# Kernel optimization log

Measured on AMD Instinct MI355X. Metric: run time of the kernel, lower is better.

The kernel has to match this reference:

```python
import jax, jax.numpy as jnp
import numpy as np

D_MODEL = 256
NUM_HEADS = 8
DEPTH = D_MODEL // NUM_HEADS
CITY_SEQ = 2048
B = 4
SQ = 2048
EPS = 1e-9
WEIGHTING = 'IDW'  # branch used (Linear/IDW/Gaussian in original)


def setup_inputs() -> dict:
    key = jax.random.key(0)
    ks = jax.random.split(key, 12)
    s = 1.0 / np.sqrt(D_MODEL)
    return {
        'query': jax.random.normal(ks[0], (B, SQ, D_MODEL), jnp.float32),
        'values': jax.random.normal(ks[1], (B, SQ, D_MODEL), jnp.float32),
        'distance_matrix': jax.random.uniform(ks[2], (B, SQ, CITY_SEQ), jnp.float32),
        'Wq_w': jax.random.normal(ks[3], (D_MODEL, D_MODEL), jnp.float32) * s,
        'Wq_b': jnp.zeros((D_MODEL,), jnp.float32),
        'Wk_w': jax.random.normal(ks[4], (D_MODEL, D_MODEL), jnp.float32) * s,
        'Wk_b': jnp.zeros((D_MODEL,), jnp.float32),
        'Wv_w': jax.random.normal(ks[5], (D_MODEL, D_MODEL), jnp.float32) * s,
        'Wv_b': jnp.zeros((D_MODEL,), jnp.float32),
        'fc_w': jax.random.normal(ks[6], (D_MODEL, D_MODEL), jnp.float32) * s,
        'fc_b': jnp.zeros((D_MODEL,), jnp.float32),
        'trainable_keys': jax.random.normal(ks[7], (CITY_SEQ, D_MODEL), jnp.float32),
    }


def _distance_weights(dist):
    # IDW branch: per-row normalized inverse distance, shape [B, Sq, S]
    inv = 1.0 / (dist + EPS)
    return inv / jnp.sum(inv, axis=-1, keepdims=True)


def reference(query, values, distance_matrix, Wq_w, Wq_b, Wk_w, Wk_b,
              Wv_w, Wv_b, fc_w, fc_b, trainable_keys):
    b = query.shape[0]
    q = query @ Wq_w.T + Wq_b                      # [B, Sq, D]
    k = trainable_keys @ Wk_w.T + Wk_b             # [S, D] (shared across batch)
    v = values @ Wv_w.T + Wv_b                     # [B, S, D]

    qh = q.reshape(b, -1, NUM_HEADS, DEPTH)        # [B, Sq, H, d]
    kh = k.reshape(-1, NUM_HEADS, DEPTH)           # [S, H, d]
    vh = v.reshape(b, -1, NUM_HEADS, DEPTH)        # [B, S, H, d]

    scale = 1.0 / jnp.sqrt(jnp.asarray(DEPTH, jnp.float32))
    scores = jnp.einsum('bqhd,khd->bhqk', qh, kh) * scale   # [B, H, Sq, S]
    dw = _distance_weights(distance_matrix)[:, None, :, :]  # [B, 1, Sq, S]
    scores = scores * dw
    attn = jax.nn.softmax(scores, axis=-1)
    out = jnp.einsum('bhqk,bkhd->bqhd', attn, vh).reshape(b, -1, D_MODEL)
    return out @ fc_w.T + fc_b
```

## Files before the change

kernel.cpp:

```cpp
#include <hip/hip_runtime.h>

#define BB 4
#define SQn 2048
#define SS 2048
#define DM 256
#define DH 32

typedef unsigned short u16;
typedef unsigned int u32;
typedef _Float16 f16;
typedef __attribute__((ext_vector_type(8))) f16 f16x8;
typedef __attribute__((ext_vector_type(8))) short s16x8;
typedef __attribute__((ext_vector_type(4))) float f32x4;
typedef __attribute__((ext_vector_type(2))) float f32x2;
typedef __attribute__((ext_vector_type(4))) u32 u32x4;
typedef __attribute__((ext_vector_type(2))) u32 u32x2;

__device__ __forceinline__ float bf2f(u16 x){ u32 u=((u32)x)<<16; return __builtin_bit_cast(float,u); }
__device__ __forceinline__ u16 f2bf(float f){ u32 u=__builtin_bit_cast(u32,f); u32 r=(u+0x7fffu+((u>>16)&1u))>>16; return (u16)r; }

__device__ __forceinline__ f16x8 ld8(const void* p, size_t off, int fl)
{
    f16x8 r;
    if (fl) {
        const float* f = (const float*)p + off;
        f32x4 a = *(const f32x4*)f;
        f32x4 b = *(const f32x4*)(f + 4);
        #pragma unroll
        for (int i = 0; i < 4; ++i) { r[i] = (f16)a[i]; r[4+i] = (f16)b[i]; }
    } else {
        const u16* s = (const u16*)p + off;
        u32x4 v = *(const u32x4*)s;
        #pragma unroll
        for (int i = 0; i < 4; ++i) {
            u32 x = v[i];
            r[2*i]   = (f16)bf2f((u16)(x & 0xffff));
            r[2*i+1] = (f16)bf2f((u16)(x >> 16));
        }
    }
    return r;
}
__device__ __forceinline__ float ld1(const void* p, int idx, int fl)
{ return fl ? ((const float*)p)[idx] : bf2f(((const u16*)p)[idx]); }

__global__ void detect_kernel(const u32* __restrict__ q, int* __restrict__ flag)
{
    int t = threadIdx.x;
    u32 w = q[t];
    u32 e = (w >> 7) & 0xFFu;
    int vote = ((e >= 0x70u && e <= 0x85u) || ((w & 0xFFFFu) == 0u)) ? 1 : 0;
    #pragma unroll
    for (int d = 1; d < 64; d <<= 1) vote += __shfl_xor(vote, d);
    __shared__ int ps[4];
    if ((t & 63) == 0) ps[t >> 6] = vote;
    __syncthreads();
    if (t == 0) *flag = ((ps[0]+ps[1]+ps[2]+ps[3]) >= 128) ? 0 : 1;
}

__global__ __launch_bounds__(256) void proj_kernel(
    const int* __restrict__ flag,
    const void* __restrict__ query, const void* __restrict__ values, const void* __restrict__ tkeys,
    const void* __restrict__ Wq, const void* __restrict__ Wqb,
    const void* __restrict__ Wk, const void* __restrict__ Wkb,
    const void* __restrict__ Wv, const void* __restrict__ Wvb,
    f16* __restrict__ qf, f16* __restrict__ kf, u16* __restrict__ vt)
{
    int fl = *flag;
    int bx = blockIdx.x;
    const void *X, *W, *Bi; int mode, rowbase;
    if (bx < 128)      { X=query;  W=Wq; Bi=Wqb; mode=0; rowbase=bx*64; }
    else if (bx < 256) { X=values; W=Wv; Bi=Wvb; mode=2; rowbase=(bx-128)*64; }
    else               { X=tkeys;  W=Wk; Bi=Wkb; mode=1; rowbase=(bx-256)*64; }
    int colbase = blockIdx.y * 64;

    __shared__ f16 Xs[64][40];
    __shared__ f16 Ws[64][40];
    __shared__ u16 Os[64][72];

    int t = threadIdx.x;
    int lane = t & 63, w = t >> 6;
    int quad = lane >> 4, l15 = lane & 15;

    const f32x4 fz = {0.f,0.f,0.f,0.f};
    f32x4 acc[4] = {fz,fz,fz,fz};

    for (int ks = 0; ks < 8; ++ks) {
        int k0 = ks * 32;
        {
            int row = t >> 2, ch = (t & 3) * 8;
            f16x8 xv = ld8(X, (size_t)(rowbase+row)*DM + k0 + ch, fl);
            f16x8 wv = ld8(W, (size_t)(colbase+row)*DM + k0 + ch, fl);
            *(f16x8*)(&Xs[row][ch]) = xv;
            *(f16x8*)(&Ws[row][ch]) = wv;
        }
        __syncthreads();
        f16x8 a = *(const f16x8*)(&Xs[w*16 + l15][quad*8]);
        #pragma unroll
        for (int nt = 0; nt < 4; ++nt) {
            f16x8 bfr = *(const f16x8*)(&Ws[nt*16 + l15][quad*8]);
            acc[nt] = __builtin_amdgcn_mfma_f32_16x16x32_f16(a, bfr, acc[nt], 0, 0, 0);
        }
        __syncthreads();
    }

    if (mode == 2) {
        int m = rowbase + w*16 + quad*4;
        int bb = m >> 11, s = m & 2047;
        int ktv = s >> 5, qv = (s >> 3) & 3, kk = s & 7;
        #pragma unroll
        for (int nt = 0; nt < 4; ++nt) {
            int col = colbase + nt*16 + l15;
            float bv = ld1(Bi, col, fl);
            int hv = col >> 5, ntv = (col >> 4) & 1;
            size_t idx = (((((size_t)(bb*8 + hv))*64 + ktv)*2 + ntv)*4 + qv)*128
                         + (size_t)(col & 15)*8 + kk;
            u32x2 pk;
            pk[0] = (u32)f2bf(acc[nt][0]+bv) | ((u32)f2bf(acc[nt][1]+bv) << 16);
            pk[1] = (u32)f2bf(acc[nt][2]+bv) | ((u32)f2bf(acc[nt][3]+bv) << 16);
            *(u32x2*)(vt + idx) = pk;
        }
    } else {
        #pragma unroll
        for (int nt = 0; nt < 4; ++nt) {
            int col = nt*16 + l15;
            float bv = ld1(Bi, colbase + col, fl);
            #pragma unroll
            for (int r = 0; r < 4; ++r)
                Os[w*16 + quad*4 + r][col] = __builtin_bit_cast(u16, (f16)(acc[nt][r] + bv));
        }
        __syncthreads();
        #pragma unroll
        for (int p = 0; p < 2; ++p) {
            int rr = (t >> 3) + p*32;
            int ch = (t & 7) * 8;
            u32x4 v = *(const u32x4*)(&Os[rr][ch]);
            if (mode == 0) {
                *(u32x4*)(qf + (size_t)(rowbase+rr)*DM + colbase + ch) = v;
            } else {
                int head = (colbase + ch) >> 5;
                int dh = ch & 31;
                *(u32x4*)(kf + (size_t)head*(SS*DH) + (size_t)(rowbase+rr)*DH + dh) = v;
            }
        }
    }
}

__global__ __launch_bounds__(256) void dwsum_kernel(
    const int* __restrict__ flag, const void* __restrict__ dist, float* __restrict__ distT)
{
    int fl = *flag;
    int row = blockIdx.x;
    int t = threadIdx.x;

    float d[8];
    if (fl) {
        const float* p = (const float*)dist + (size_t)row * SS + t*8;
        f32x4 a = *(const f32x4*)p;
        f32x4 b4 = *(const f32x4*)(p + 4);
        #pragma unroll
        for (int i = 0; i < 4; ++i) { d[i] = a[i]; d[4+i] = b4[i]; }
    } else {
        const u16* p = (const u16*)dist + (size_t)row * SS + t*8;
        u32x4 v = *(const u32x4*)p;
        #pragma unroll
        for (int i = 0; i < 4; ++i) {
            u32 x = v[i];
            d[2*i]   = bf2f((u16)(x & 0xffff));
            d[2*i+1] = bf2f((u16)(x >> 16));
        }
    }
    float s = 0.f;
    #pragma unroll
    for (int i = 0; i < 8; ++i) s += 1.0f / (d[i] + 1e-9f);
    #pragma unroll
    for (int dd = 1; dd < 64; dd <<= 1) s += __shfl_xor(s, dd);
    __shared__ float ps[4];
    __shared__ float srs;
    if ((t & 63) == 0) ps[t >> 6] = s;
    __syncthreads();
    if (t == 0) srs = 0.17677669529663687f / (ps[0] + ps[1] + ps[2] + ps[3]);
    __syncthreads();
    float rs = srs;

    int b = row >> 11, q = row & 2047;
    int qt = q >> 5, mt = (q >> 4) & 1, l15 = q & 15;
    #pragma unroll
    for (int c = 0; c < 2; ++c) {
        int k = t*8 + c*4;
        int kt = k >> 5, nt = (k >> 4) & 1, quad = (k >> 2) & 3;
        f32x4 wv;
        #pragma unroll
        for (int r = 0; r < 4; ++r)
            wv[r] = rs * __builtin_amdgcn_rcpf(d[c*4 + r] + 1e-9f);
        size_t idx = ((size_t)((b*64 + qt)*64 + kt))*1024
                     + (mt*2 + nt)*256 + (quad*16 + l15)*4;
        *(f32x4*)(distT + idx) = wv;
    }
}

#define LDP 40
#define LDO 264
#define DB_OFF 40960
#define OL_OFF  49152
#define OUTF_OFF 66048

__global__ __launch_bounds__(1024) void attn_kernel(
    const int* __restrict__ flag,
    const float* __restrict__ distT,
    const f16* __restrict__ qf, const f16* __restrict__ kf, const u16* __restrict__ vtg,
    const void* __restrict__ fcw, const void* __restrict__ fcb,
    void* __restrict__ out)
{
    __shared__ __align__(16) char smem[99840];

    int fl = *flag;
    int t = threadIdx.x;
    int w = t >> 6, lane = t & 63;
    int quad = lane >> 4, l15 = lane & 15;
    int b = blockIdx.y, q0 = blockIdx.x * 32;
    int h = w & 7, khalf = w >> 3;

    u16* Pw = (u16*)(smem + w * 2560);
    float* dbB = (float*)(smem + DB_OFF);

    f16x8 aq[2];
    #pragma unroll
    for (int mt = 0; mt < 2; ++mt)
        aq[mt] = *(const f16x8*)(qf + (size_t)(b*SQn + q0 + mt*16 + l15)*DM + h*DH + quad*8);

    u32 ov = (l15 == 0) ? 0x3F803F80u : 0u;
    u32x4 ovv = {ov, ov, ov, ov};
    s16x8 ones = __builtin_bit_cast(s16x8, ovv);

    const f32x4 fz = {0.f,0.f,0.f,0.f};
    f32x4 o[2][2] = {{fz,fz},{fz,fz}};
    f32x4 lacc[2] = {fz, fz};

    const f16* kfh = kf + (size_t)h * (SS*DH);
    const u16* vth = vtg + (((size_t)(b*8 + h)) << 16);
    const float* dTb = distT + ((size_t)(b*64 + blockIdx.x))*64*1024;

    int g  = t >> 9;
    int tt = t & 511;

    {
        f32x2 sv = *(const f32x2*)(dTb + (size_t)(g*32)*1024 + tt*2);
        float* d0 = dbB + g*1024;
        *(f32x2*)(d0 + tt*2) = sv;
    }
    f16x8 ck[2]; s16x8 cv[2];
    {
        int ktg0 = khalf * 32;
        #pragma unroll
        for (int nt = 0; nt < 2; ++nt) {
            ck[nt] = *(const f16x8*)(kfh + (size_t)(ktg0*32 + nt*16 + l15)*DH + quad*8);
            cv[nt] = __builtin_bit_cast(s16x8,
                *(const u32x4*)(vth + (size_t)ktg0*1024 + nt*512 + quad*128 + l15*8));
        }
    }
    __syncthreads();

    for (int kt = 0; kt < 32; ++kt) {
        int ktn  = (kt + 1) & 31;
        int ktgn = khalf*32 + ktn;

        f32x2 sv = *(const f32x2*)(dTb + (size_t)(g*32 + ktn)*1024 + tt*2);
        f16x8 nk[2]; s16x8 nv[2];
        #pragma unroll
        for (int nt = 0; nt < 2; ++nt) {
            nk[nt] = *(const f16x8*)(kfh + (size_t)(ktgn*32 + nt*16 + l15)*DH + quad*8);
            nv[nt] = __builtin_bit_cast(s16x8,
                *(const u32x4*)(vth + (size_t)ktgn*1024 + nt*512 + quad*128 + l15*8));
        }

        const float* dbc = dbB + ((kt & 1)*2 + khalf)*1024;
        f32x4 dd[2][2];
        #pragma unroll
        for (int mt = 0; mt < 2; ++mt)
            #pragma unroll
            for (int nt = 0; nt < 2; ++nt)
                dd[mt][nt] = *(const f32x4*)(dbc + (mt*2 + nt)*256 + lane*4);

        f32x4 st[2][2];
        #pragma unroll
        for (int mt = 0; mt < 2; ++mt)
            #pragma unroll
            for (int nt = 0; nt < 2; ++nt)
                st[mt][nt] = __builtin_amdgcn_mfma_f32_16x16x32_f16(ck[nt], aq[mt], fz, 0, 0, 0);

        #pragma unroll
        for (int mt = 0; mt < 2; ++mt)
            #pragma unroll
            for (int nt = 0; nt < 2; ++nt) {
                u32 pb[4];
                #pragma unroll
                for (int r = 0; r < 4; ++r) {
                    float p = __expf(st[mt][nt][r] * dd[mt][nt][r]);
                    pb[r] = __builtin_bit_cast(u32, p);
                }
                u32x2 pk;
                pk[0] = __builtin_amdgcn_perm(pb[1], pb[0], 0x07060302u);
                pk[1] = __builtin_amdgcn_perm(pb[3], pb[2], 0x07060302u);
                *(u32x2*)(Pw + (mt*16 + l15)*LDP + nt*16 + quad*4) = pk;
            }
        __asm__ __volatile__("" ::: "memory");

        #pragma unroll
        for (int mt = 0; mt < 2; ++mt) {
            s16x8 ap = *(const s16x8*)(Pw + (mt*16 + l15)*LDP + quad*8);
            lacc[mt] = __builtin_amdgcn_mfma_f32_16x16x32_bf16(ap, ones, lacc[mt], 0, 0, 0);
            #pragma unroll
            for (int nt = 0; nt < 2; ++nt)
                o[mt][nt] = __builtin_amdgcn_mfma_f32_16x16x32_bf16(ap, cv[nt], o[mt][nt], 0, 0, 0);
        }

        {
            float* dbn = dbB + (((kt + 1) & 1)*2 + g)*1024;
            *(f32x2*)(dbn + tt*2) = sv;
        }
        __syncthreads();

        ck[0] = nk[0]; ck[1] = nk[1]; cv[0] = nv[0]; cv[1] = nv[1];
    }

    float* Cx = (float*)smem;
    if (w >= 8) {
        float* dst = Cx + ((w - 8)*64 + lane)*24;
        *(f32x4*)(dst +  0) = o[0][0];
        *(f32x4*)(dst +  4) = o[0][1];
        *(f32x4*)(dst +  8) = o[1][0];
        *(f32x4*)(dst + 12) = o[1][1];
        *(f32x4*)(dst + 16) = lacc[0];
        *(f32x4*)(dst + 20) = lacc[1];
    }
    __syncthreads();
    f16* Ol = (f16*)(smem + OL_OFF);
    if (w < 8) {
        const float* src = Cx + (w*64 + lane)*24;
        o[0][0] += *(const f32x4*)(src +  0);
        o[0][1] += *(const f32x4*)(src +  4);
        o[1][0] += *(const f32x4*)(src +  8);
        o[1][1] += *(const f32x4*)(src + 12);
        lacc[0] += *(const f32x4*)(src + 16);
        lacc[1] += *(const f32x4*)(src + 20);

        #pragma unroll
        for (int mt = 0; mt < 2; ++mt)
            #pragma unroll
            for (int r = 0; r < 4; ++r) {
                float lv = __shfl(lacc[mt][r], lane & 48);
                float inv = 1.0f / lv;
                o[mt][0][r] *= inv;
                o[mt][1][r] *= inv;
            }

        #pragma unroll
        for (int mt = 0; mt < 2; ++mt)
            #pragma unroll
            for (int nt = 0; nt < 2; ++nt)
                #pragma unroll
                for (int r = 0; r < 4; ++r)
                    Ol[(mt*16 + quad*4 + r)*LDO + h*DH + nt*16 + l15] = (f16)o[mt][nt][r];
    }
    __syncthreads();

    f32x4 c[2] = {fz, fz};
    int n = w*16 + l15;
    for (int ks = 0; ks < 8; ++ks) {
        f16x8 bw = ld8(fcw, (size_t)n*DM + ks*32 + quad*8, fl);
        #pragma unroll
        for (int mt = 0; mt < 2; ++mt) {
            f16x8 a2 = *(const f16x8*)(Ol + (mt*16 + l15)*LDO + ks*32 + quad*8);
            c[mt] = __builtin_amdgcn_mfma_f32_16x16x32_f16(a2, bw, c[mt], 0, 0, 0);
        }
    }
    float* OutF = (float*)(smem + OUTF_OFF);
    {
        float bv = ld1(fcb, n, fl);
        #pragma unroll
        for (int mt = 0; mt < 2; ++mt)
            #pragma unroll
            for (int r = 0; r < 4; ++r)
                OutF[(mt*16 + quad*4 + r)*LDO + n] = c[mt][r] + bv;
    }
    __syncthreads();
    if (fl) {
        float* of = (float*)out;
        int row = t >> 5, col = (t & 31) * 8;
        f32x4 v0 = *(const f32x4*)(OutF + row*LDO + col);
        f32x4 v1 = *(const f32x4*)(OutF + row*LDO + col + 4);
        float* dst = of + ((size_t)(b*SQn + q0 + row))*DM + col;
        *(f32x4*)dst       = v0;
        *(f32x4*)(dst + 4) = v1;
    } else {
        u16* ob = (u16*)out;
        int row = t >> 5, col = (t & 31) * 8;
        f32x4 v0 = *(const f32x4*)(OutF + row*LDO + col);
        f32x4 v1 = *(const f32x4*)(OutF + row*LDO + col + 4);
        u32x4 pk;
        pk[0] = (u32)f2bf(v0[0]) | ((u32)f2bf(v0[1]) << 16);
        pk[1] = (u32)f2bf(v0[2]) | ((u32)f2bf(v0[3]) << 16);
        pk[2] = (u32)f2bf(v1[0]) | ((u32)f2bf(v1[1]) << 16);
        pk[3] = (u32)f2bf(v1[2]) | ((u32)f2bf(v1[3]) << 16);
        *(u32x4*)(ob + ((size_t)(b*SQn + q0 + row))*DM + col) = pk;
    }
}

extern "C" void kernel_launch(void* const* d_in, const int* in_sizes, int n_in,
                              void* d_out, int out_size, void* d_ws, size_t ws_size,
                              hipStream_t stream)
{
    const void* query  = d_in[0];
    const void* values = d_in[1];
    const void* dist   = d_in[2];
    const void* Wq     = d_in[3];
    const void* Wqb    = d_in[4];
    const void* Wk     = d_in[5];
    const void* Wkb    = d_in[6];
    const void* Wv     = d_in[7];
    const void* Wvb    = d_in[8];
    const void* fcw    = d_in[9];
    const void* fcb    = d_in[10];
    const void* tkeys  = d_in[11];

    char* ws   = (char*)d_ws;
    f16*  qf   = (f16*)ws;
    f16*  kf   = (f16*)(ws + (4u << 20));
    u16*  vt   = (u16*)(ws + (5u << 20));
    int*  flag = (int*)(ws + (9u << 20));
    float* dT  = (float*)(ws + (16u << 20));

    detect_kernel<<<1, 256, 0, stream>>>((const u32*)query, flag);
    proj_kernel<<<dim3(288, 4), 256, 0, stream>>>(flag, query, values, tkeys,
                                                  Wq, Wqb, Wk, Wkb, Wv, Wvb,
                                                  qf, kf, vt);
    dwsum_kernel<<<dim3(BB * SQn), 256, 0, stream>>>(flag, dist, dT);
    attn_kernel<<<dim3(64, 4), 1024, 0, stream>>>(flag, dT, qf, kf, vt, fcw, fcb, d_out);
}
```

Before: 236.0 us.

## Store distance weights as fp16 in a padded row-major tile layout

```diff
diff --git a/kernel.cpp b/kernel.cpp
--- a/kernel.cpp
+++ b/kernel.cpp
@@ -10,6 +10,7 @@
 typedef unsigned int u32;
 typedef _Float16 f16;
 typedef __attribute__((ext_vector_type(8))) f16 f16x8;
+typedef __attribute__((ext_vector_type(4))) f16 f16x4;
 typedef __attribute__((ext_vector_type(8))) short s16x8;
 typedef __attribute__((ext_vector_type(4))) float f32x4;
 typedef __attribute__((ext_vector_type(2))) float f32x2;
@@ -146,7 +147,7 @@
 }
 
 __global__ __launch_bounds__(256) void dwsum_kernel(
-    const int* __restrict__ flag, const void* __restrict__ dist, float* __restrict__ distT)
+    const int* __restrict__ flag, const void* __restrict__ dist, u16* __restrict__ distT)
 {
     int fl = *flag;
     int row = blockIdx.x;
@@ -183,30 +184,27 @@
     float rs = srs;
 
     int b = row >> 11, q = row & 2047;
-    int qt = q >> 5, mt = (q >> 4) & 1, l15 = q & 15;
+    int qt = q >> 5, ql = q & 31;
+    size_t base = ((size_t)((b*64 + qt)*64 + (t >> 2)))*1024 + ql*32 + (t & 3)*8;
+    u32x4 pk;
     #pragma unroll
-    for (int c = 0; c < 2; ++c) {
-        int k = t*8 + c*4;
-        int kt = k >> 5, nt = (k >> 4) & 1, quad = (k >> 2) & 3;
-        f32x4 wv;
-        #pragma unroll
-        for (int r = 0; r < 4; ++r)
-            wv[r] = rs * __builtin_amdgcn_rcpf(d[c*4 + r] + 1e-9f);
-        size_t idx = ((size_t)((b*64 + qt)*64 + kt))*1024
-                     + (mt*2 + nt)*256 + (quad*16 + l15)*4;
-        *(f32x4*)(distT + idx) = wv;
-    }
+    for (int i = 0; i < 4; ++i) {
+        u16 lo = __builtin_bit_cast(u16, (f16)(rs * __builtin_amdgcn_rcpf(d[2*i]   + 1e-9f)));
+        u16 hi = __builtin_bit_cast(u16, (f16)(rs * __builtin_amdgcn_rcpf(d[2*i+1] + 1e-9f)));
+        pk[i] = (u32)lo | ((u32)hi << 16);
+    }
+    *(u32x4*)(distT + base) = pk;
 }
 
 #define LDP 40
 #define LDO 264
-#define DB_OFF 40960
+#define DB_OFF 53248
 #define OL_OFF  49152
 #define OUTF_OFF 66048
 
 __global__ __launch_bounds__(1024) void attn_kernel(
     const int* __restrict__ flag,
-    const float* __restrict__ distT,
+    const u16* __restrict__ distT,
     const f16* __restrict__ qf, const f16* __restrict__ kf, const u16* __restrict__ vtg,
     const void* __restrict__ fcw, const void* __restrict__ fcb,
     void* __restrict__ out)
@@ -221,7 +219,7 @@
     int h = w & 7, khalf = w >> 3;
 
     u16* Pw = (u16*)(smem + w * 2560);
-    float* dbB = (float*)(smem + DB_OFF);
+    u16* dbU = (u16*)(smem + DB_OFF);
 
     f16x8 aq[2];
     #pragma unroll
@@ -238,15 +236,15 @@
 
     const f16* kfh = kf + (size_t)h * (SS*DH);
     const u16* vth = vtg + (((size_t)(b*8 + h)) << 16);
-    const float* dTb = distT + ((size_t)(b*64 + blockIdx.x))*64*1024;
+    const u16* dTb = distT + ((size_t)(b*64 + blockIdx.x))*64*1024;
 
     int g  = t >> 9;
     int tt = t & 511;
+    int drow = tt >> 4, dcol = (tt & 15)*2;
 
     {
-        f32x2 sv = *(const f32x2*)(dTb + (size_t)(g*32)*1024 + tt*2);
-        float* d0 = dbB + g*1024;
-        *(f32x2*)(d0 + tt*2) = sv;
+        u32 sv = *(const u32*)(dTb + (size_t)(g*32)*1024 + tt*2);
+        *(u32*)(dbU + g*1152 + drow*36 + dcol) = sv;
     }
     f16x8 ck[2]; s16x8 cv[2];
     {
@@ -264,7 +262,7 @@
         int ktn  = (kt + 1) & 31;
         int ktgn = khalf*32 + ktn;
 
-        f32x2 sv = *(const f32x2*)(dTb + (size_t)(g*32 + ktn)*1024 + tt*2);
+        u32 sv = *(const u32*)(dTb + (size_t)(g*32 + ktn)*1024 + tt*2);
         f16x8 nk[2]; s16x8 nv[2];
         #pragma unroll
         for (int nt = 0; nt < 2; ++nt) {
@@ -273,13 +271,13 @@
                 *(const u32x4*)(vth + (size_t)ktgn*1024 + nt*512 + quad*128 + l15*8));
         }
 
-        const float* dbc = dbB + ((kt & 1)*2 + khalf)*1024;
-        f32x4 dd[2][2];
+        const u16* dbc = dbU + ((kt & 1)*2 + khalf)*1152;
+        f16x4 ddh[2][2];
         #pragma unroll
         for (int mt = 0; mt < 2; ++mt)
             #pragma unroll
             for (int nt = 0; nt < 2; ++nt)
-                dd[mt][nt] = *(const f32x4*)(dbc + (mt*2 + nt)*256 + lane*4);
+                ddh[mt][nt] = *(const f16x4*)(dbc + (mt*16 + l15)*36 + nt*16 + quad*4);
 
         f32x4 st[2][2];
         #pragma unroll
@@ -295,7 +293,7 @@
                 u32 pb[4];
                 #pragma unroll
                 for (int r = 0; r < 4; ++r) {
-                    float p = __expf(st[mt][nt][r] * dd[mt][nt][r]);
+                    float p = __expf(st[mt][nt][r] * (float)ddh[mt][nt][r]);
                     pb[r] = __builtin_bit_cast(u32, p);
                 }
                 u32x2 pk;
@@ -314,10 +312,7 @@
                 o[mt][nt] = __builtin_amdgcn_mfma_f32_16x16x32_bf16(ap, cv[nt], o[mt][nt], 0, 0, 0);
         }
 
-        {
-            float* dbn = dbB + (((kt + 1) & 1)*2 + g)*1024;
-            *(f32x2*)(dbn + tt*2) = sv;
-        }
+        *(u32*)(dbU + (((kt + 1) & 1)*2 + g)*1152 + drow*36 + dcol) = sv;
         __syncthreads();
 
         ck[0] = nk[0]; ck[1] = nk[1]; cv[0] = nv[0]; cv[1] = nv[1];
@@ -428,7 +423,7 @@
     f16*  kf   = (f16*)(ws + (4u << 20));
     u16*  vt   = (u16*)(ws + (5u << 20));
     int*  flag = (int*)(ws + (9u << 20));
-    float* dT  = (float*)(ws + (16u << 20));
+    u16*  dT   = (u16*)(ws + (16u << 20));
 
     detect_kernel<<<1, 256, 0, stream>>>((const u32*)query, flag);
     proj_kernel<<<dim3(288, 4), 256, 0, stream>>>(flag, query, values, tkeys,
```

New measurement: 194.0 us. -17.8%, faster.
